# Optimization experiments

Hardware: AMD Instinct MI355X
Metric: run time of the kernel (lower is better)

Reference implementation:

```python
import jax, jax.numpy as jnp
import numpy as np

B, N, K, H, C, PE, EMB, OUT = 2, 2048, 16, 4, 8, 64, 1024, 2
P = C * (C + 1) // 2  # 36 unordered class pairs
RADIUS, NEG, EPS = 0.08, 0.2, 1e-5


def _ball_query(pos, radius, nsample):
    # pos [B,N,2] -> idx [B,N,nsample]; indices within radius, padded with first in-ball index
    sq = jnp.sum(pos * pos, -1)
    d = sq[:, :, None] + sq[:, None, :] - 2.0 * jnp.einsum('bnc,bmc->bnm', pos, pos)
    n = pos.shape[1]
    idx = jnp.broadcast_to(jnp.arange(n)[None, None, :], d.shape)
    idx = jnp.where(d > radius * radius, n, idx)
    idx = jnp.sort(idx, axis=-1)[:, :, :nsample]
    return jnp.where(idx == n, idx[:, :, :1], idx)


def _gather(feat, idx):
    # feat [B,F,N], idx [B,N,K] -> [B,F,N,K]
    return jnp.take_along_axis(feat[:, :, None, :], idx[:, None, :, :], axis=3)


def _pe(rel, dim):
    # sinusoidal encoding of relative coords rel [B,2,N,K] -> [B,dim,N,K]
    nf = dim // 4
    freqs = 10000.0 ** (-jnp.arange(nf, dtype=rel.dtype) / nf)
    ang = rel[:, :, None] * freqs[None, None, :, None, None]     # [B,2,nf,N,K]
    enc = jnp.concatenate([jnp.sin(ang), jnp.cos(ang)], axis=2)  # [B,2,2nf,N,K]
    b = enc.shape[0]
    return enc.reshape(b, dim, enc.shape[3], enc.shape[4])


def _conv(x, w, g, bvec):
    # 1x1 conv (no bias) + inference BN (running mean 0, var 1) + LeakyReLU
    y = jnp.einsum('oc,bc...->bo...', w, x) / jnp.sqrt(1.0 + EPS)
    sh = (1, -1) + (1,) * (y.ndim - 2)
    return jax.nn.leaky_relu(y * g.reshape(sh) + bvec.reshape(sh), NEG)


def _attn_layer(x, Ws, a_pairs, a_selfs, core, tgt):
    # PointpairAttentionLayer (per-class-pair coefficients), vmapped over heads.
    # x [B,F,N,K]; core [B,N] int; tgt [B,N,K] int
    s0 = jnp.minimum(tgt, core[:, :, None])
    s1 = jnp.maximum(tgt, core[:, :, None])
    pidx = s0 * C - (s0 * (s0 - 1)) // 2 + (s1 - s0)             # [B,N,K] pair index
    self_mask = (tgt[:, :, 0] < core)[:, :, None]                # slot-0 keeps a_self when pair-write happened earlier

    def head(W, a_pair, a_self):
        Wh = jnp.einsum('bfnk,fg->bnkg', x, W)                   # [B,N,K,F]
        a = a_pair[pidx]                                         # [B,N,K,F]
        slot0 = jnp.where(self_mask, a_self[core], a[:, :, 0])
        a = a.at[:, :, 0].set(slot0)
        e = jax.nn.leaky_relu(Wh * a, NEG)
        attn = jax.nn.softmax(e, axis=2)                         # over K neighbors
        return jax.nn.elu(attn * Wh)                             # [B,N,K,F]

    hs = jax.vmap(head)(Ws, a_pairs, a_selfs)                    # [H,B,N,K,F]
    b, n, k = x.shape[0], x.shape[2], x.shape[3]
    return jnp.transpose(hs, (1, 0, 4, 2, 3)).reshape(b, -1, n, k)


def _edge(feat, idx):
    # DGCNN edge features: concat(neighbor - center, center)
    tf = _gather(feat, idx)
    return jnp.concatenate([tf - feat[..., None],
                            jnp.broadcast_to(feat[..., None], tf.shape)], axis=1)


def _forward(pos, types, conv1_w, bn1_g, bn1_b, W1, ap1, as1,
             conv2_w, bn2_g, bn2_b, W2, ap2, as2,
             conv3_w, bn3_g, bn3_b, W3, ap3, as3,
             conv4_w, bn4_g, bn4_b, W4, ap4, as4,
             conv5_w, bn5_g, bn5_b, lin1_w, bn6_g, bn6_b,
             lin2_w, lin2_b, bn7_g, bn7_b, lin3_w, lin3_b):
    idx = _ball_query(pos, RADIUS, K)                            # [B,N,K]
    posT = jnp.transpose(pos, (0, 2, 1))                         # [B,2,N]
    rel = _gather(posT, idx) - posT[..., None]                   # [B,2,N,K]
    tgt = _gather(types[:, None, :], idx)[:, 0]                  # [B,N,K] neighbor classes

    x = _conv(_pe(rel, PE), conv1_w, bn1_g, bn1_b)               # [B,64,N,K]
    x1 = _attn_layer(x, W1, ap1, as1, types, tgt).sum(-1)        # [B,H*64,N]
    x = _conv(_edge(x1, idx), conv2_w, bn2_g, bn2_b)             # [B,64,N,K]
    x2 = _attn_layer(x, W2, ap2, as2, types, tgt).sum(-1)        # [B,H*64,N]
    x = _conv(_edge(x2, idx), conv3_w, bn3_g, bn3_b)             # [B,128,N,K]
    x3 = _attn_layer(x, W3, ap3, as3, types, tgt).sum(-1)        # [B,H*128,N]
    x = _conv(_edge(x3, idx), conv4_w, bn4_g, bn4_b)             # [B,256,N,K]
    x4 = _attn_layer(x, W4, ap4, as4, types, tgt).sum(-1)        # [B,H*256,N]

    xc = jnp.concatenate([x1, x2, x3, x4], axis=1)               # [B,H*512,N]
    x = _conv(xc, conv5_w, bn5_g, bn5_b)                         # [B,EMB,N]
    feat = jnp.concatenate([x.max(-1), x.mean(-1)], axis=-1)     # [B,2*EMB]

    def bn1d(y, g, bvec):
        return (y / jnp.sqrt(1.0 + EPS)) * g + bvec

    h = jax.nn.leaky_relu(bn1d(feat @ lin1_w.T, bn6_g, bn6_b), NEG)
    h = jax.nn.leaky_relu(bn1d(h @ lin2_w.T + lin2_b, bn7_g, bn7_b), NEG)
    return h @ lin3_w.T + lin3_b                                 # [B,OUT]


def setup_inputs() -> dict:
    key = jax.random.key(0)
    ks = iter(jax.random.split(key, 64))
    rn = lambda *s: jax.random.normal(next(ks), s, dtype=jnp.float32)
    d = {}
    d['pos'] = jax.random.uniform(next(ks), (B, N, 2), dtype=jnp.float32)
    d['types'] = jax.random.randint(next(ks), (B, N), 0, C, dtype=jnp.int32)

    def layer(f_in, f, tag):
        d['conv%d_w' % tag] = rn(f, f_in) * (1.0 / np.sqrt(f_in))
        d['bn%d_g' % tag] = jnp.ones((f,), jnp.float32)
        d['bn%d_b' % tag] = jnp.zeros((f,), jnp.float32)

    layer(PE, 64, 1)
    d['W1'] = rn(H, 64, 64) * 0.125; d['ap1'] = rn(H, P, 64) * 0.5; d['as1'] = rn(H, C, 64) * 0.5
    layer(2 * H * 64, 64, 2)
    d['W2'] = rn(H, 64, 64) * 0.125; d['ap2'] = rn(H, P, 64) * 0.5; d['as2'] = rn(H, C, 64) * 0.5
    layer(2 * H * 64, 128, 3)
    d['W3'] = rn(H, 128, 128) * 0.09; d['ap3'] = rn(H, P, 128) * 0.5; d['as3'] = rn(H, C, 128) * 0.5
    layer(2 * H * 128, 256, 4)
    d['W4'] = rn(H, 256, 256) * 0.0625; d['ap4'] = rn(H, P, 256) * 0.5; d['as4'] = rn(H, C, 256) * 0.5
    layer(H * 512, EMB, 5)
    d['lin1_w'] = rn(512, 2 * EMB) * 0.02
    d['bn6_g'] = jnp.ones((512,), jnp.float32); d['bn6_b'] = jnp.zeros((512,), jnp.float32)
    d['lin2_w'] = rn(256, 512) * 0.04; d['lin2_b'] = jnp.zeros((256,), jnp.float32)
    d['bn7_g'] = jnp.ones((256,), jnp.float32); d['bn7_b'] = jnp.zeros((256,), jnp.float32)
    d['lin3_w'] = rn(OUT, 256) * 0.06; d['lin3_b'] = jnp.zeros((OUT,), jnp.float32)
    return d


def reference(pos, types, conv1_w, bn1_g, bn1_b, W1, ap1, as1,
              conv2_w, bn2_g, bn2_b, W2, ap2, as2,
              conv3_w, bn3_g, bn3_b, W3, ap3, as3,
              conv4_w, bn4_g, bn4_b, W4, ap4, as4,
              conv5_w, bn5_g, bn5_b, lin1_w, bn6_g, bn6_b,
              lin2_w, lin2_b, bn7_g, bn7_b, lin3_w, lin3_b):
    return _forward(pos, types, conv1_w, bn1_g, bn1_b, W1, ap1, as1,
                    conv2_w, bn2_g, bn2_b, W2, ap2, as2,
                    conv3_w, bn3_g, bn3_b, W3, ap3, as3,
                    conv4_w, bn4_g, bn4_b, W4, ap4, as4,
                    conv5_w, bn5_g, bn5_b, lin1_w, bn6_g, bn6_b,
                    lin2_w, lin2_b, bn7_g, bn7_b, lin3_w, lin3_b)
```

## Files before the change

### kernel.cpp

```cpp
#include <hip/hip_runtime.h>
#include <math.h>

#define BB 2
#define NN 2048
#define KK 16
#define HH 4
#define CC 8
#define PP 36
#define NEGS 0.2f
#define INVS 0.9999950000374997f

typedef __attribute__((ext_vector_type(8))) short s16x8;
typedef __attribute__((ext_vector_type(8))) unsigned short u16x8;
typedef __attribute__((ext_vector_type(4))) float f32x4;

__device__ inline unsigned short bfh(float x) {
  unsigned u = __float_as_uint(x);
  return (unsigned short)((u + 0x7FFFu + ((u >> 16) & 1u)) >> 16);
}
__device__ inline float bff(unsigned short h) {
  return __uint_as_float(((unsigned)h) << 16);
}
__device__ inline f32x4 mfma16(s16x8 a, s16x8 b, f32x4 c) {
  return __builtin_amdgcn_mfma_f32_16x16x32_bf16(a, b, c, 0, 0, 0);
}

__global__ __launch_bounds__(256) void k_ballquery(const float* __restrict__ pos,
                                                   const int* __restrict__ types,
                                                   int* __restrict__ idxg,
                                                   int* __restrict__ acode,
                                                   float* __restrict__ rel) {
  __shared__ int s_buf[4][KK];
  const float r2 = (float)(0.08 * 0.08);
  int wslot = threadIdx.x >> 6;
  int lane = threadIdx.x & 63;
  int wg = blockIdx.x * 4 + wslot;
  int b = wg / NN, n = wg - b * NN;
  const float* pb = pos + (size_t)b * NN * 2;
  float px = pb[n * 2 + 0], py = pb[n * 2 + 1];
  float sqn = px * px + py * py;
  unsigned mask = 0u;
  int base = lane * 32;
  for (int j = 0; j < 32; ++j) {
    float qx = pb[(base + j) * 2 + 0], qy = pb[(base + j) * 2 + 1];
    float sqm = qx * qx + qy * qy;
    float d = sqn + sqm - 2.0f * (px * qx + py * qy);
    if (d <= r2) mask |= (1u << j);
  }
  int cnt = __popc(mask);
  int inc = cnt;
#pragma unroll
  for (int off = 1; off < 64; off <<= 1) {
    int v = __shfl_up(inc, off, 64);
    if (lane >= off) inc += v;
  }
  int total = __shfl(inc, 63, 64);
  int excl = inc - cnt;
  unsigned mm = mask;
  int p = excl;
  while (mm && p < KK) {
    int j = __ffs(mm) - 1;
    mm &= mm - 1u;
    s_buf[wslot][p] = base + j;
    ++p;
  }
  __syncthreads();
  int tc = total < KK ? total : KK;
  if (lane < KK) {
    int m0 = s_buf[wslot][0];
    int mk = (lane < tc) ? s_buf[wslot][lane] : m0;
    idxg[wg * KK + lane] = mk;
    int core = types[b * NN + n];
    int tg = types[b * NN + mk];
    int s0 = tg < core ? tg : core;
    int s1 = tg < core ? core : tg;
    int code = s0 * CC - (s0 * (s0 - 1)) / 2 + (s1 - s0);
    if (lane == 0 && tg < core) code = PP + core;
    acode[wg * KK + lane] = code;
    rel[(wg * KK + lane) * 2 + 0] = pb[mk * 2 + 0] - px;
    rel[(wg * KK + lane) * 2 + 1] = pb[mk * 2 + 1] - py;
  }
}

struct PackDesc {
  const float* src;
  unsigned short* dh;
  unsigned short* dl;
  int KB, NT, srcld, Cdiff, mode, sstride, dstride, nrep, bpr;
};
struct PackArgs {
  PackDesc d[20];
};
__global__ __launch_bounds__(256) void k_megapack(PackArgs pa) {
  PackDesc D = pa.d[blockIdx.y];
  int rep = blockIdx.x / D.bpr;
  if (rep >= D.nrep) return;
  int f = (blockIdx.x - rep * D.bpr) * 256 + threadIdx.x;
  int total = D.KB * D.NT * 64;
  if (f >= total) return;
  const float* src = D.src + (size_t)rep * D.sstride;
  unsigned short* dh = D.dh + (size_t)rep * D.dstride;
  if (D.mode == 3) {
    if (f * 8 >= D.Cdiff) return;
    float* dd = (float*)dh;
    size_t o = (size_t)f * 8;
#pragma unroll
    for (int i = 0; i < 8; ++i) dd[o + i] = src[o + i];
    return;
  }
  unsigned short* dl = D.dl + (size_t)rep * D.dstride;
  int l = f & 63;
  int t2 = f >> 6;
  int n = (t2 / D.KB) * 16 + (l & 15);
  int k0 = (t2 % D.KB) * 32 + ((l >> 4) * 8);
  size_t o = (size_t)t2 * 512 + (size_t)l * 8;
#pragma unroll
  for (int i = 0; i < 8; ++i) {
    int k = k0 + i;
    float v;
    if (D.mode == 0) {
      v = src[(size_t)k * D.srcld + n];
    } else if (D.mode == 1) {
      v = src[(size_t)n * D.srcld + k];
    } else {
      v = src[(size_t)n * D.srcld + k + D.Cdiff] - src[(size_t)n * D.srcld + k];
    }
    unsigned short hi = bfh(v);
    dh[o + i] = hi;
    dl[o + i] = bfh(v - bff(hi));
  }
}

template <int KBW, int NTB>
__global__ __launch_bounds__(512, 4) void k_pregemm(
    const unsigned short* __restrict__ xh, int xoff,
    const unsigned short* __restrict__ wph, const unsigned short* __restrict__ wpl,
    const float* __restrict__ scale, const float* __restrict__ bias,
    float* __restrict__ ouv, int cout) {
  constexpr int NCH = KBW / 2;
  constexpr int JT = NTB / 2;
  const int ld = 2 * cout;
  __shared__ alignas(16) char s_mem[32768];
  int tid = threadIdx.x;
  int lane = tid & 63;
  int w = tid >> 6;
  int lg = lane >> 4;
  int ln = lane & 15;
  int bm = blockIdx.x;
  int ntoff = blockIdx.y * NTB;
  int wm = w >> 1, wn = w & 1;
  f32x4 acc[2][JT];
#pragma unroll
  for (int m = 0; m < 2; ++m)
#pragma unroll
    for (int j = 0; j < JT; ++j) acc[m][j] = (f32x4){0.f, 0.f, 0.f, 0.f};

  int srowg = bm * 128 + w * 16 + ln;
  const unsigned short* gH = xh + (size_t)srowg * 2048 + xoff + lg * 8;
  int wbyA = ((w * 2 + 0) * 64 + lane) * 16;
  int wbyB = ((w * 2 + 1) * 64 + lane) * 16;
  u16x8 h0, h1;
  auto load2 = [&](int ch) {
    h0 = *(const u16x8*)(gH + ch * 64);
    h1 = *(const u16x8*)(gH + ch * 64 + 32);
  };
  load2(0);
  *(u16x8*)(s_mem + wbyA) = h0;
  *(u16x8*)(s_mem + wbyB) = h1;
  __syncthreads();
  int p = 0;
  for (int ch = 0; ch < NCH; ++ch) {
    if (ch + 1 < NCH) load2(ch + 1);
#pragma unroll
    for (int ks = 0; ks < 2; ++ks) {
      s16x8 ah[2];
#pragma unroll
      for (int m = 0; m < 2; ++m) {
        int by = p * 16384 + (((wm * 2 + m) * 2 + ks) * 64 + lane) * 16;
        ah[m] = *(const s16x8*)(s_mem + by);
      }
      int kb = ch * 2 + ks;
      __builtin_amdgcn_s_setprio(1);
#pragma unroll
      for (int j = 0; j < JT; ++j) {
        size_t fo = ((size_t)(ntoff + wn * JT + j) * KBW + kb) * 64 + lane;
        s16x8 bh = ((const s16x8*)wph)[fo];
        s16x8 bl = ((const s16x8*)wpl)[fo];
#pragma unroll
        for (int m = 0; m < 2; ++m) {
          acc[m][j] = mfma16(ah[m], bh, acc[m][j]);
          acc[m][j] = mfma16(ah[m], bl, acc[m][j]);
        }
      }
      __builtin_amdgcn_s_setprio(0);
    }
    if (ch + 1 < NCH) {
      int d = (p ^ 1) * 16384;
      *(u16x8*)(s_mem + d + wbyA) = h0;
      *(u16x8*)(s_mem + d + wbyB) = h1;
      p ^= 1;
    }
    __syncthreads();
  }
#pragma unroll
  for (int j = 0; j < JT; ++j) {
    int g = (ntoff + wn * JT + j) * 16 + ln;
    int gm = g >= cout ? g - cout : g;
    float sc = scale[gm] * INVS;
    float bs = (g >= cout) ? bias[gm] : 0.f;
#pragma unroll
    for (int m = 0; m < 2; ++m) {
#pragma unroll
      for (int reg = 0; reg < 4; ++reg) {
        int row = bm * 128 + wm * 32 + m * 16 + lg * 4 + reg;
        ouv[(size_t)row * ld + g] = acc[m][j][reg] * sc + bs;
      }
    }
  }
}

template <int FOUT, int MT>
__device__ __forceinline__ void attn_phase(
    const char* s_mem, const int* s_code, unsigned short* xh, int pgbase,
    int w, int lane, const unsigned short* __restrict__ attnh,
    const unsigned short* __restrict__ attnl, const float* __restrict__ coef,
    int ooff) {
  constexpr int KBA = FOUT / 32;
  constexpr int NT = FOUT / 16;
  constexpr int NTW_A = NT / 2;
  constexpr int JW = (MT == 8) ? 1 : ((NTW_A > 2) ? 2 : NTW_A);
  constexpr int NPASS = NTW_A / JW;
  int lg = lane >> 4;
  int ln = lane & 15;
  int h = w >> 1, nh = w & 1;
  const s16x8* wph = (const s16x8*)(attnh + (size_t)h * FOUT * FOUT);
  const s16x8* wpl = (const s16x8*)(attnl + (size_t)h * FOUT * FOUT);
  const float* hb = coef + (size_t)h * 44 * FOUT + ln;
#pragma unroll 1
  for (int pass = 0; pass < NPASS; ++pass) {
    float ac[MT][JW][4];
#pragma unroll
    for (int m = 0; m < MT; ++m)
#pragma unroll
      for (int reg = 0; reg < 4; ++reg) {
        int off = s_code[m * 16 + lg * 4 + reg] * FOUT;
#pragma unroll
        for (int j = 0; j < JW; ++j) {
          int nt = nh * NTW_A + pass * JW + j;
          ac[m][j][reg] = hb[off + nt * 16];
        }
      }
    f32x4 aacc[MT][JW];
#pragma unroll
    for (int m = 0; m < MT; ++m)
#pragma unroll
      for (int j = 0; j < JW; ++j) aacc[m][j] = (f32x4){0.f, 0.f, 0.f, 0.f};
#pragma unroll 2
    for (int kb = 0; kb < KBA; ++kb) {
      s16x8 ah[MT];
#pragma unroll
      for (int m = 0; m < MT; ++m) {
        int by = ((m * KBA + kb) * 64 + lane) * 16;
        ah[m] = *(const s16x8*)(s_mem + by);
      }
      __builtin_amdgcn_s_setprio(1);
#pragma unroll
      for (int j = 0; j < JW; ++j) {
        int nt = nh * NTW_A + pass * JW + j;
        size_t fo = ((size_t)nt * KBA + kb) * 64 + lane;
        s16x8 bh = wph[fo];
        s16x8 bl = wpl[fo];
#pragma unroll
        for (int m = 0; m < MT; ++m) {
          aacc[m][j] = mfma16(ah[m], bh, aacc[m][j]);
          aacc[m][j] = mfma16(ah[m], bl, aacc[m][j]);
        }
      }
      __builtin_amdgcn_s_setprio(0);
    }
#pragma unroll
    for (int m = 0; m < MT; ++m) {
      int pg = pgbase + m;
#pragma unroll
      for (int j = 0; j < JW; ++j) {
        int nt = nh * NTW_A + pass * JW + j;
        int g = nt * 16 + ln;
        float e[4];
        float ssum = 0.f;
#pragma unroll
        for (int reg = 0; reg < 4; ++reg) {
          float ev = aacc[m][j][reg] * ac[m][j][reg];
          ev = (ev >= 0.f) ? ev : NEGS * ev;
          float pe = __expf(ev);
          e[reg] = pe;
          ssum += pe;
        }
        ssum += __shfl_xor(ssum, 16, 64);
        ssum += __shfl_xor(ssum, 32, 64);
        float inv = 1.f / ssum;
        float o = 0.f;
#pragma unroll
        for (int reg = 0; reg < 4; ++reg) {
          float u = e[reg] * inv * aacc[m][j][reg];
          o += (u > 0.f) ? u : (__expf(u) - 1.f);
        }
        o += __shfl_xor(o, 16, 64);
        o += __shfl_xor(o, 32, 64);
        if (lane < 16) {
          xh[(size_t)pg * 2048 + ooff + h * FOUT + g] = bfh(o);
        }
      }
    }
  }
}

template <int FOUT>
__global__ __launch_bounds__(512, 4) void k_attn(
    unsigned short* xh, const float* __restrict__ uv,
    const int* __restrict__ idx, const int* __restrict__ acode,
    const unsigned short* __restrict__ attnh, const unsigned short* __restrict__ attnl,
    const float* __restrict__ coef, int ooff) {
  constexpr int MT = 8;
  constexpr int KBA = FOUT / 32;
  constexpr int YPLANE = MT * 16 * FOUT * 2;
  constexpr int FPW = (MT * KBA) / 8;
  constexpr int C2 = 2 * FOUT;

  __shared__ alignas(16) char s_mem[YPLANE];
  __shared__ int s_gsrc[MT * 16];
  __shared__ int s_code[MT * 16];

  int tid = threadIdx.x;
  int lane = tid & 63;
  int w = tid >> 6;
  int lg = lane >> 4;
  int ln = lane & 15;
  int pgbase = blockIdx.x * MT;

  if (tid < MT * 16) {
    int pg = pgbase + (tid >> 4);
    int b = pg >> 11;
    s_gsrc[tid] = b * 2048 + idx[pg * KK + (tid & 15)];
    s_code[tid] = acode[pg * KK + (tid & 15)];
  }
  __syncthreads();

#pragma unroll
  for (int r = 0; r < FPW; ++r) {
    int f = w * FPW + r;
    int mt = f / KBA, kb = f % KBA;
    int row = mt * 16 + ln;
    int col = kb * 32 + lg * 8;
    const float* up = uv + (size_t)s_gsrc[row] * C2 + col;
    const float* cp = uv + (size_t)(pgbase + mt) * C2 + FOUT + col;
    float4 u0 = *(const float4*)up;
    float4 u1 = *(const float4*)(up + 4);
    float4 v0 = *(const float4*)cp;
    float4 v1 = *(const float4*)(cp + 4);
    float uu[8] = {u0.x, u0.y, u0.z, u0.w, u1.x, u1.y, u1.z, u1.w};
    float vv[8] = {v0.x, v0.y, v0.z, v0.w, v1.x, v1.y, v1.z, v1.w};
    unsigned short oh[8];
#pragma unroll
    for (int i = 0; i < 8; ++i) {
      float t = uu[i] + vv[i];
      t = (t >= 0.f) ? t : NEGS * t;
      oh[i] = bfh(t);
    }
    *(u16x8*)(s_mem + (f * 64 + lane) * 16) = *(u16x8*)oh;
  }
  __syncthreads();

  attn_phase<FOUT, MT>(s_mem, s_code, xh, pgbase, w, lane, attnh, attnl, coef, ooff);
}

__global__ __launch_bounds__(512, 4) void k_layer1(
    unsigned short* xh, const float* __restrict__ rel, const int* __restrict__ idx,
    const int* __restrict__ acode,
    const unsigned short* __restrict__ convh, const unsigned short* __restrict__ convl,
    const unsigned short* __restrict__ attnh, const unsigned short* __restrict__ attnl,
    const float* __restrict__ bng, const float* __restrict__ bnb,
    const float* __restrict__ coef, int ooff) {
  constexpr int FOUT = 64;
  constexpr int KB = 2;
  constexpr int KBA = 2;
  constexpr int YPLANE = 64 * FOUT * 2;

  __shared__ alignas(16) char s_mem[YPLANE];
  __shared__ int s_gsrc[64];
  __shared__ int s_code[64];

  int tid = threadIdx.x;
  int lane = tid & 63;
  int w = tid >> 6;
  int lg = lane >> 4;
  int ln = lane & 15;
  int pgbase = blockIdx.x * 4;

  if (tid < 64) {
    int pg = pgbase + (tid >> 4);
    int b = pg >> 11;
    s_gsrc[tid] = b * 2048 + idx[pg * KK + (tid & 15)];
    s_code[tid] = acode[pg * KK + (tid & 15)];
  }
  __syncthreads();

  {
    int smt = w >> 1, skb = w & 1;
    float rc = rel[((size_t)(pgbase + smt) * KK + ln) * 2 + skb];
    unsigned short hb[8];
#pragma unroll
    for (int i = 0; i < 8; ++i) {
      int j = lg * 8 + i;
      int fidx = j & 15;
      float freq = exp2f(-(float)fidx * 0.8304820237218406f);
      float ang = rc * freq;
      float v = (j < 16) ? __sinf(ang) : __cosf(ang);
      hb[i] = bfh(v);
    }
    *(u16x8*)(s_mem + ((w * 64 + lane) * 16)) = *(u16x8*)hb;
  }
  __syncthreads();

  int wr = w >> 2, wc = w & 3;
  f32x4 cacc[2];
  cacc[0] = (f32x4){0.f, 0.f, 0.f, 0.f};
  cacc[1] = (f32x4){0.f, 0.f, 0.f, 0.f};
#pragma unroll
  for (int ks = 0; ks < 2; ++ks) {
    s16x8 ah[2];
#pragma unroll
    for (int m = 0; m < 2; ++m) {
      int by = (((wr * 2 + m) * 2 + ks) * 64 + lane) * 16;
      ah[m] = *(const s16x8*)(s_mem + by);
    }
    __builtin_amdgcn_s_setprio(1);
    size_t fo = ((size_t)wc * KB + ks) * 64 + lane;
    s16x8 bh = ((const s16x8*)convh)[fo];
    s16x8 bl = ((const s16x8*)convl)[fo];
#pragma unroll
    for (int m = 0; m < 2; ++m) {
      cacc[m] = mfma16(ah[m], bh, cacc[m]);
      cacc[m] = mfma16(ah[m], bl, cacc[m]);
    }
    __builtin_amdgcn_s_setprio(0);
  }
  __syncthreads();

  {
    int g = wc * 16 + ln;
    float sc = bng[g] * INVS;
    float bs = bnb[g];
    int gpart = ((g >> 5) * 64 + ((g >> 3) & 3) * 16) * 16 + (g & 7) * 2;
#pragma unroll
    for (int m = 0; m < 2; ++m) {
#pragma unroll
      for (int reg = 0; reg < 4; ++reg) {
        int r = wr * 32 + m * 16 + lg * 4 + reg;
        float v = cacc[m][reg] * sc + bs;
        v = (v >= 0.f) ? v : NEGS * v;
        int by = (r >> 4) * (KBA * 1024) + gpart + (r & 15) * 16;
        *(unsigned short*)(s_mem + by) = bfh(v);
      }
    }
  }
  __syncthreads();

  attn_phase<64, 4>(s_mem, s_code, xh, pgbase, w, lane, attnh, attnl, coef, ooff);
}

__global__ __launch_bounds__(512, 2) void k_gemm5_m(const unsigned short* __restrict__ xh,
                                                    const unsigned short* __restrict__ bph,
                                                    const unsigned short* __restrict__ bpl,
                                                    const float* __restrict__ g5,
                                                    const float* __restrict__ b5,
                                                    float* __restrict__ pmax,
                                                    float* __restrict__ psum) {
  __shared__ alignas(16) char s_mem[65536];
  int tid = threadIdx.x;
  int lane = tid & 63;
  int w = tid >> 6;
  int lg = lane >> 4;
  int ln = lane & 15;
  int bm = blockIdx.x, bn = blockIdx.y;
  int wm = w >> 2, wn = w & 3;
  f32x4 acc[8];
#pragma unroll
  for (int m = 0; m < 8; ++m) acc[m] = (f32x4){0.f, 0.f, 0.f, 0.f};

  int sr = w * 16 + ln;
  const unsigned short* gH = xh + (size_t)(bm * 256 + sr) * 2048 + lg * 8;
  const unsigned short* gH2 = gH + (size_t)128 * 2048;
  int fm = sr >> 4;
  int fl = lg * 16 + (sr & 15);
  int wbyA = ((fm * 2 + 0) * 64 + fl) * 16;
  int wbyB = ((fm * 2 + 1) * 64 + fl) * 16;
  int wbyC = (((fm + 8) * 2 + 0) * 64 + fl) * 16;
  int wbyD = (((fm + 8) * 2 + 1) * 64 + fl) * 16;
  u16x8 h0, h1, h2, h3;
  auto load4 = [&](int ch) {
    h0 = *(const u16x8*)(gH + ch * 64);
    h1 = *(const u16x8*)(gH + ch * 64 + 32);
    h2 = *(const u16x8*)(gH2 + ch * 64);
    h3 = *(const u16x8*)(gH2 + ch * 64 + 32);
  };
  load4(0);
  *(u16x8*)(s_mem + wbyA) = h0;
  *(u16x8*)(s_mem + wbyB) = h1;
  *(u16x8*)(s_mem + wbyC) = h2;
  *(u16x8*)(s_mem + wbyD) = h3;
  __syncthreads();
  int p = 0;
  for (int ch = 0; ch < 32; ++ch) {
    if (ch + 1 < 32) load4(ch + 1);
#pragma unroll
    for (int ks = 0; ks < 2; ++ks) {
      s16x8 ah[8];
#pragma unroll
      for (int m = 0; m < 8; ++m) {
        int by = p * 32768 + (((wm * 8 + m) * 2 + ks) * 64 + lane) * 16;
        ah[m] = *(const s16x8*)(s_mem + by);
      }
      int kb = ch * 2 + ks;
      __builtin_amdgcn_s_setprio(1);
      {
        size_t fo = ((size_t)(bn * 4 + wn) * 64 + kb) * 64 + lane;
        s16x8 bh = ((const s16x8*)bph)[fo];
        s16x8 bl = ((const s16x8*)bpl)[fo];
#pragma unroll
        for (int m = 0; m < 8; ++m) {
          acc[m] = mfma16(ah[m], bh, acc[m]);
          acc[m] = mfma16(ah[m], bl, acc[m]);
        }
      }
      __builtin_amdgcn_s_setprio(0);
    }
    if (ch + 1 < 32) {
      int d = (p ^ 1) * 32768;
      *(u16x8*)(s_mem + d + wbyA) = h0;
      *(u16x8*)(s_mem + d + wbyB) = h1;
      *(u16x8*)(s_mem + d + wbyC) = h2;
      *(u16x8*)(s_mem + d + wbyD) = h3;
      p ^= 1;
    }
    __syncthreads();
  }

  float cmax, csum;
  {
    int g = bn * 64 + wn * 16 + ln;
    float sc = g5[g] * INVS;
    float bs = b5[g];
    float mx = -3.0e38f, sm = 0.f;
#pragma unroll
    for (int m = 0; m < 8; ++m)
#pragma unroll
      for (int reg = 0; reg < 4; ++reg) {
        float v = acc[m][reg] * sc + bs;
        v = (v >= 0.f) ? v : NEGS * v;
        mx = fmaxf(mx, v);
        sm += v;
      }
    mx = fmaxf(mx, __shfl_xor(mx, 16, 64));
    mx = fmaxf(mx, __shfl_xor(mx, 32, 64));
    sm += __shfl_xor(sm, 16, 64);
    sm += __shfl_xor(sm, 32, 64);
    cmax = mx;
    csum = sm;
  }
  float* s_f = (float*)s_mem;
  if (lg == 0) {
    int col = wn * 16 + ln;
    s_f[(wm * 64 + col) * 2 + 0] = cmax;
    s_f[(wm * 64 + col) * 2 + 1] = csum;
  }
  __syncthreads();
  if (tid < 64) {
    float mx = fmaxf(s_f[tid * 2], s_f[(64 + tid) * 2]);
    float sm = s_f[tid * 2 + 1] + s_f[(64 + tid) * 2 + 1];
    pmax[(size_t)bm * 1024 + bn * 64 + tid] = mx;
    psum[(size_t)bm * 1024 + bn * 64 + tid] = sm;
  }
}

__global__ __launch_bounds__(256) void k_feat(const float* __restrict__ pmax,
                                              const float* __restrict__ psum,
                                              float* __restrict__ feat) {
  int t = blockIdx.x * 256 + threadIdx.x;
  if (t >= BB * 1024) return;
  int b = t >> 10, o = t & 1023;
  float mx = -3.0e38f, sm = 0.f;
  for (int i = 0; i < 8; ++i) {
    mx = fmaxf(mx, pmax[(size_t)(b * 8 + i) * 1024 + o]);
    sm += psum[(size_t)(b * 8 + i) * 1024 + o];
  }
  feat[b * 2048 + o] = mx;
  feat[b * 2048 + 1024 + o] = sm * (1.0f / NN);
}

template <bool HASB, bool DOBN, bool ACT>
__global__ __launch_bounds__(256) void k_head(const float* __restrict__ X,
                                              const float* __restrict__ Wm,
                                              const float* __restrict__ bias,
                                              const float* __restrict__ g,
                                              const float* __restrict__ bb,
                                              float* __restrict__ Y, int IN, int ON) {
  int gt = blockIdx.x * 256 + threadIdx.x;
  int w = gt >> 6, lane = gt & 63;
  if (w >= BB * ON) return;
  int b = w / ON, o = w - b * ON;
  const float* x = X + (size_t)b * IN;
  const float* wr = Wm + (size_t)o * IN;
  float s = 0.f;
  for (int c = lane; c < IN; c += 64) s += x[c] * wr[c];
#pragma unroll
  for (int off = 32; off > 0; off >>= 1) s += __shfl_down(s, off, 64);
  if (lane == 0) {
    if (HASB) s += bias[o];
    if (DOBN) s = s * INVS * g[o] + bb[o];
    if (ACT) s = (s >= 0.f) ? s : NEGS * s;
    Y[(size_t)b * ON + o] = s;
  }
}

extern "C" void kernel_launch(void* const* d_in, const int* in_sizes, int n_in,
                              void* d_out, int out_size, void* d_ws, size_t ws_size,
                              hipStream_t stream) {
  const float* pos = (const float*)d_in[0];
  const int* types = (const int*)d_in[1];
  const float* conv1_w = (const float*)d_in[2];
  const float* bn1_g = (const float*)d_in[3];
  const float* bn1_b = (const float*)d_in[4];
  const float* W1 = (const float*)d_in[5];
  const float* ap1 = (const float*)d_in[6];
  const float* as1 = (const float*)d_in[7];
  const float* conv2_w = (const float*)d_in[8];
  const float* bn2_g = (const float*)d_in[9];
  const float* bn2_b = (const float*)d_in[10];
  const float* W2 = (const float*)d_in[11];
  const float* ap2 = (const float*)d_in[12];
  const float* as2 = (const float*)d_in[13];
  const float* conv3_w = (const float*)d_in[14];
  const float* bn3_g = (const float*)d_in[15];
  const float* bn3_b = (const float*)d_in[16];
  const float* W3 = (const float*)d_in[17];
  const float* ap3 = (const float*)d_in[18];
  const float* as3 = (const float*)d_in[19];
  const float* conv4_w = (const float*)d_in[20];
  const float* bn4_g = (const float*)d_in[21];
  const float* bn4_b = (const float*)d_in[22];
  const float* W4 = (const float*)d_in[23];
  const float* ap4 = (const float*)d_in[24];
  const float* as4 = (const float*)d_in[25];
  const float* conv5_w = (const float*)d_in[26];
  const float* bn5_g = (const float*)d_in[27];
  const float* bn5_b = (const float*)d_in[28];
  const float* lin1_w = (const float*)d_in[29];
  const float* bn6_g = (const float*)d_in[30];
  const float* bn6_b = (const float*)d_in[31];
  const float* lin2_w = (const float*)d_in[32];
  const float* lin2_b = (const float*)d_in[33];
  const float* bn7_g = (const float*)d_in[34];
  const float* bn7_b = (const float*)d_in[35];
  const float* lin3_w = (const float*)d_in[36];
  const float* lin3_b = (const float*)d_in[37];
  (void)in_sizes; (void)n_in; (void)out_size; (void)ws_size;

  float* ws = (float*)d_ws;
  size_t off = 0;
  auto take = [&](size_t nf) {
    float* p = ws + off;
    off += (nf + 63) & ~(size_t)63;
    return p;
  };
  auto takeu = [&](size_t nu) { return (unsigned short*)take((nu + 1) / 2); };

  int* idx = (int*)take(BB * NN * KK);
  int* acode = (int*)take(BB * NN * KK);
  float* rel = take((size_t)BB * NN * KK * 2);
  unsigned short* xh = takeu((size_t)BB * NN * 2048);
  float* uv = take((size_t)4096 * 512);
  float* pmax = take(16 * 1024);
  float* psum = take(16 * 1024);
  float* feat = take(BB * 2048);
  float* h1 = take(BB * 512);
  float* h2 = take(BB * 256);
  unsigned short* c1h = takeu(64 * 64);
  unsigned short* c1l = takeu(64 * 64);
  unsigned short* uvw2h = takeu(256 * 128);
  unsigned short* uvw2l = takeu(256 * 128);
  unsigned short* uvw3h = takeu(256 * 256);
  unsigned short* uvw3l = takeu(256 * 256);
  unsigned short* uvw4h = takeu(512 * 512);
  unsigned short* uvw4l = takeu(512 * 512);
  unsigned short* a1h = takeu(4 * 64 * 64);
  unsigned short* a1l = takeu(4 * 64 * 64);
  unsigned short* a2h = takeu(4 * 64 * 64);
  unsigned short* a2l = takeu(4 * 64 * 64);
  unsigned short* a3h = takeu(4 * 128 * 128);
  unsigned short* a3l = takeu(4 * 128 * 128);
  unsigned short* a4h = takeu(4 * 256 * 256);
  unsigned short* a4l = takeu(4 * 256 * 256);
  unsigned short* g5h = takeu((size_t)2048 * 1024);
  unsigned short* g5l = takeu((size_t)2048 * 1024);
  float* coef1 = take(4 * 44 * 64);
  float* coef2 = take(4 * 44 * 64);
  float* coef3 = take(4 * 44 * 128);
  float* coef4 = take(4 * 44 * 256);

  dim3 blk(256);
  dim3 blk5(512);

  PackArgs pa;
  pa.d[0] = {conv1_w, c1h, c1l, 2, 4, 64, 0, 1, 0, 0, 1, 2};
  pa.d[1] = {conv2_w, uvw2h, uvw2l, 8, 4, 512, 0, 1, 0, 0, 1, 8};
  pa.d[2] = {conv2_w, uvw2h + 16384, uvw2l + 16384, 8, 4, 512, 256, 2, 0, 0, 1, 8};
  pa.d[3] = {conv3_w, uvw3h, uvw3l, 8, 8, 512, 0, 1, 0, 0, 1, 16};
  pa.d[4] = {conv3_w, uvw3h + 32768, uvw3l + 32768, 8, 8, 512, 256, 2, 0, 0, 1, 16};
  pa.d[5] = {conv4_w, uvw4h, uvw4l, 16, 16, 1024, 0, 1, 0, 0, 1, 64};
  pa.d[6] = {conv4_w, uvw4h + 131072, uvw4l + 131072, 16, 16, 1024, 512, 2, 0, 0, 1, 64};
  pa.d[7] = {W1, a1h, a1l, 2, 4, 64, 0, 0, 4096, 4096, 4, 2};
  pa.d[8] = {W2, a2h, a2l, 2, 4, 64, 0, 0, 4096, 4096, 4, 2};
  pa.d[9] = {W3, a3h, a3l, 4, 8, 128, 0, 0, 16384, 16384, 4, 8};
  pa.d[10] = {W4, a4h, a4l, 8, 16, 256, 0, 0, 65536, 65536, 4, 32};
  pa.d[11] = {conv5_w, g5h, g5l, 64, 64, 2048, 0, 1, 0, 0, 1, 1024};
  pa.d[12] = {ap1, (unsigned short*)coef1, nullptr, 5, 1, 0, 2304, 3, 2304, 5632, 4, 2};
  pa.d[13] = {as1, (unsigned short*)(coef1 + 2304), nullptr, 1, 1, 0, 512, 3, 512, 5632, 4, 1};
  pa.d[14] = {ap2, (unsigned short*)coef2, nullptr, 5, 1, 0, 2304, 3, 2304, 5632, 4, 2};
  pa.d[15] = {as2, (unsigned short*)(coef2 + 2304), nullptr, 1, 1, 0, 512, 3, 512, 5632, 4, 1};
  pa.d[16] = {ap3, (unsigned short*)coef3, nullptr, 9, 1, 0, 4608, 3, 4608, 11264, 4, 3};
  pa.d[17] = {as3, (unsigned short*)(coef3 + 4608), nullptr, 2, 1, 0, 1024, 3, 1024, 11264, 4, 1};
  pa.d[18] = {ap4, (unsigned short*)coef4, nullptr, 18, 1, 0, 9216, 3, 9216, 22528, 4, 5};
  pa.d[19] = {as4, (unsigned short*)(coef4 + 9216), nullptr, 4, 1, 0, 2048, 3, 2048, 22528, 4, 1};
  k_megapack<<<dim3(1024, 20), blk, 0, stream>>>(pa);

  k_ballquery<<<dim3(BB * NN / 4), blk, 0, stream>>>(pos, types, idx, acode, rel);

  k_layer1<<<dim3(BB * NN / 4), blk5, 0, stream>>>(
      xh, rel, idx, acode, c1h, c1l, a1h, a1l, bn1_g, bn1_b, coef1, 0);

  k_pregemm<8, 4><<<dim3(32, 2), blk5, 0, stream>>>(
      xh, 0, uvw2h, uvw2l, bn2_g, bn2_b, uv, 64);
  k_attn<64><<<dim3(BB * NN / 8), blk5, 0, stream>>>(
      xh, uv, idx, acode, a2h, a2l, coef2, 256);

  k_pregemm<8, 8><<<dim3(32, 2), blk5, 0, stream>>>(
      xh, 256, uvw3h, uvw3l, bn3_g, bn3_b, uv, 128);
  k_attn<128><<<dim3(BB * NN / 8), blk5, 0, stream>>>(
      xh, uv, idx, acode, a3h, a3l, coef3, 512);

  k_pregemm<16, 8><<<dim3(32, 4), blk5, 0, stream>>>(
      xh, 512, uvw4h, uvw4l, bn4_g, bn4_b, uv, 256);
  k_attn<256><<<dim3(BB * NN / 8), blk5, 0, stream>>>(
      xh, uv, idx, acode, a4h, a4l, coef4, 1024);

  k_gemm5_m<<<dim3(16, 16), blk5, 0, stream>>>(xh, g5h, g5l, bn5_g, bn5_b, pmax, psum);
  k_feat<<<dim3(8), blk, 0, stream>>>(pmax, psum, feat);
  k_head<false, true, true><<<dim3(BB * 512 * 64 / 256), blk, 0, stream>>>(
      feat, lin1_w, nullptr, bn6_g, bn6_b, h1, 2048, 512);
  k_head<true, true, true><<<dim3(BB * 256 * 64 / 256), blk, 0, stream>>>(
      h1, lin2_w, lin2_b, bn7_g, bn7_b, h2, 512, 256);
  k_head<true, false, false><<<dim3(1), blk, 0, stream>>>(
      h2, lin3_w, lin3_b, nullptr, nullptr, (float*)d_out, 256, 2);
}
```

Measured before the change: 349.5 us.

## Switch attention GEMMs to 32x32x16 MFMA with 4-point blocks

Replaces the 16x16x32 bf16 MFMA attention phase with a 32x32x16 variant, changing the LDS operand layout, the weight packing (a new pack mode for 32-wide column tiles) and the softmax epilogue to match the 32x32 accumulator layout. Attention blocks now process 4 points instead of 8, which doubles the grid size. The aim is fewer MFMA instructions and less weight traffic per output column, plus more blocks in flight. The cost is half the weight reuse across points per block and per-element coefficient gathers in the epilogue.

```diff
diff --git a/kernel.cpp b/kernel.cpp
--- a/kernel.cpp
+++ b/kernel.cpp
@@ -13,6 +13,7 @@
 typedef __attribute__((ext_vector_type(8))) short s16x8;
 typedef __attribute__((ext_vector_type(8))) unsigned short u16x8;
 typedef __attribute__((ext_vector_type(4))) float f32x4;
+typedef __attribute__((ext_vector_type(16))) float f32x16;
 
 __device__ inline unsigned short bfh(float x) {
   unsigned u = __float_as_uint(x);
@@ -23,6 +24,9 @@
 }
 __device__ inline f32x4 mfma16(s16x8 a, s16x8 b, f32x4 c) {
   return __builtin_amdgcn_mfma_f32_16x16x32_bf16(a, b, c, 0, 0, 0);
+}
+__device__ inline f32x16 mfma32(s16x8 a, s16x8 b, f32x16 c) {
+  return __builtin_amdgcn_mfma_f32_32x32x16_bf16(a, b, c, 0, 0, 0);
 }
 
 __global__ __launch_bounds__(256) void k_ballquery(const float* __restrict__ pos,
@@ -111,9 +115,22 @@
   unsigned short* dl = D.dl + (size_t)rep * D.dstride;
   int l = f & 63;
   int t2 = f >> 6;
+  size_t o = (size_t)t2 * 512 + (size_t)l * 8;
+  if (D.mode == 4) {
+    int nt = t2 / D.KB, ks = t2 - nt * D.KB;
+    int n = nt * 32 + (l & 31);
+    int k0 = ks * 16 + ((l >> 5) * 8);
+#pragma unroll
+    for (int i = 0; i < 8; ++i) {
+      float v = src[(size_t)(k0 + i) * D.srcld + n];
+      unsigned short hi = bfh(v);
+      dh[o + i] = hi;
+      dl[o + i] = bfh(v - bff(hi));
+    }
+    return;
+  }
   int n = (t2 / D.KB) * 16 + (l & 15);
   int k0 = (t2 % D.KB) * 32 + ((l >> 4) * 8);
-  size_t o = (size_t)t2 * 512 + (size_t)l * 8;
 #pragma unroll
   for (int i = 0; i < 8; ++i) {
     int k = k0 + i;
@@ -219,97 +236,77 @@
   }
 }
 
-template <int FOUT, int MT>
-__device__ __forceinline__ void attn_phase(
+template <int FOUT>
+__device__ __forceinline__ void attn_phase32(
     const char* s_mem, const int* s_code, unsigned short* xh, int pgbase,
     int w, int lane, const unsigned short* __restrict__ attnh,
     const unsigned short* __restrict__ attnl, const float* __restrict__ coef,
     int ooff) {
-  constexpr int KBA = FOUT / 32;
-  constexpr int NT = FOUT / 16;
-  constexpr int NTW_A = NT / 2;
-  constexpr int JW = (MT == 8) ? 1 : ((NTW_A > 2) ? 2 : NTW_A);
-  constexpr int NPASS = NTW_A / JW;
-  int lg = lane >> 4;
-  int ln = lane & 15;
+  constexpr int KS = FOUT / 16;
+  constexpr int NPASS = FOUT / 64;
+  int hi = lane >> 5;
+  int c31 = lane & 31;
   int h = w >> 1, nh = w & 1;
   const s16x8* wph = (const s16x8*)(attnh + (size_t)h * FOUT * FOUT);
   const s16x8* wpl = (const s16x8*)(attnl + (size_t)h * FOUT * FOUT);
-  const float* hb = coef + (size_t)h * 44 * FOUT + ln;
+  const float* hb = coef + (size_t)h * 44 * FOUT;
 #pragma unroll 1
   for (int pass = 0; pass < NPASS; ++pass) {
-    float ac[MT][JW][4];
-#pragma unroll
-    for (int m = 0; m < MT; ++m)
-#pragma unroll
-      for (int reg = 0; reg < 4; ++reg) {
-        int off = s_code[m * 16 + lg * 4 + reg] * FOUT;
-#pragma unroll
-        for (int j = 0; j < JW; ++j) {
-          int nt = nh * NTW_A + pass * JW + j;
-          ac[m][j][reg] = hb[off + nt * 16];
-        }
-      }
-    f32x4 aacc[MT][JW];
-#pragma unroll
-    for (int m = 0; m < MT; ++m)
-#pragma unroll
-      for (int j = 0; j < JW; ++j) aacc[m][j] = (f32x4){0.f, 0.f, 0.f, 0.f};
+    int nt32 = nh * NPASS + pass;
+    int g = nt32 * 32 + c31;
+    f32x16 acc0, acc1;
+#pragma unroll
+    for (int i = 0; i < 16; ++i) {
+      acc0[i] = 0.f;
+      acc1[i] = 0.f;
+    }
 #pragma unroll 2
-    for (int kb = 0; kb < KBA; ++kb) {
-      s16x8 ah[MT];
-#pragma unroll
-      for (int m = 0; m < MT; ++m) {
-        int by = ((m * KBA + kb) * 64 + lane) * 16;
-        ah[m] = *(const s16x8*)(s_mem + by);
-      }
+    for (int ks = 0; ks < KS; ++ks) {
+      s16x8 a0 = *(const s16x8*)(s_mem + ((0 * KS + ks) * 64 + lane) * 16);
+      s16x8 a1 = *(const s16x8*)(s_mem + ((1 * KS + ks) * 64 + lane) * 16);
+      size_t fo = ((size_t)nt32 * KS + ks) * 64 + lane;
+      s16x8 bh = wph[fo];
+      s16x8 bl = wpl[fo];
       __builtin_amdgcn_s_setprio(1);
-#pragma unroll
-      for (int j = 0; j < JW; ++j) {
-        int nt = nh * NTW_A + pass * JW + j;
-        size_t fo = ((size_t)nt * KBA + kb) * 64 + lane;
-        s16x8 bh = wph[fo];
-        s16x8 bl = wpl[fo];
-#pragma unroll
-        for (int m = 0; m < MT; ++m) {
-          aacc[m][j] = mfma16(ah[m], bh, aacc[m][j]);
-          aacc[m][j] = mfma16(ah[m], bl, aacc[m][j]);
-        }
-      }
+      acc0 = mfma32(a0, bh, acc0);
+      acc0 = mfma32(a0, bl, acc0);
+      acc1 = mfma32(a1, bh, acc1);
+      acc1 = mfma32(a1, bl, acc1);
       __builtin_amdgcn_s_setprio(0);
     }
-#pragma unroll
-    for (int m = 0; m < MT; ++m) {
-      int pg = pgbase + m;
-#pragma unroll
-      for (int j = 0; j < JW; ++j) {
-        int nt = nh * NTW_A + pass * JW + j;
-        int g = nt * 16 + ln;
-        float e[4];
-        float ssum = 0.f;
-#pragma unroll
-        for (int reg = 0; reg < 4; ++reg) {
-          float ev = aacc[m][j][reg] * ac[m][j][reg];
-          ev = (ev >= 0.f) ? ev : NEGS * ev;
-          float pe = __expf(ev);
-          e[reg] = pe;
-          ssum += pe;
-        }
-        ssum += __shfl_xor(ssum, 16, 64);
-        ssum += __shfl_xor(ssum, 32, 64);
-        float inv = 1.f / ssum;
-        float o = 0.f;
-#pragma unroll
-        for (int reg = 0; reg < 4; ++reg) {
-          float u = e[reg] * inv * aacc[m][j][reg];
-          o += (u > 0.f) ? u : (__expf(u) - 1.f);
-        }
-        o += __shfl_xor(o, 16, 64);
-        o += __shfl_xor(o, 32, 64);
-        if (lane < 16) {
-          xh[(size_t)pg * 2048 + ooff + h * FOUT + g] = bfh(o);
-        }
-      }
+#pragma unroll 1
+    for (int mt = 0; mt < 2; ++mt) {
+      const f32x16& ac = mt ? acc1 : acc0;
+      float e[16];
+      float ssA = 0.f, ssB = 0.f;
+#pragma unroll
+      for (int reg = 0; reg < 16; ++reg) {
+        int row = (reg & 3) + 8 * (reg >> 2) + 4 * hi;
+        int code = s_code[mt * 32 + row];
+        float a = hb[(size_t)code * FOUT + g];
+        float ev = ac[reg] * a;
+        ev = (ev >= 0.f) ? ev : NEGS * ev;
+        float pe = __expf(ev);
+        e[reg] = pe;
+        if (reg < 8) ssA += pe; else ssB += pe;
+      }
+      ssA += __shfl_xor(ssA, 32, 64);
+      ssB += __shfl_xor(ssB, 32, 64);
+      float invA = 1.f / ssA;
+      float invB = 1.f / ssB;
+      float oA = 0.f, oB = 0.f;
+#pragma unroll
+      for (int reg = 0; reg < 16; ++reg) {
+        float inv = (reg < 8) ? invA : invB;
+        float u = e[reg] * inv * ac[reg];
+        float t = (u > 0.f) ? u : (__expf(u) - 1.f);
+        if (reg < 8) oA += t; else oB += t;
+      }
+      oA += __shfl_xor(oA, 32, 64);
+      oB += __shfl_xor(oB, 32, 64);
+      float oS = hi ? oB : oA;
+      int pg = pgbase + mt * 2 + hi;
+      xh[(size_t)pg * 2048 + ooff + h * FOUT + g] = bfh(oS);
     }
   }
 }
@@ -320,24 +317,23 @@
     const int* __restrict__ idx, const int* __restrict__ acode,
     const unsigned short* __restrict__ attnh, const unsigned short* __restrict__ attnl,
     const float* __restrict__ coef, int ooff) {
-  constexpr int MT = 8;
-  constexpr int KBA = FOUT / 32;
-  constexpr int YPLANE = MT * 16 * FOUT * 2;
-  constexpr int FPW = (MT * KBA) / 8;
+  constexpr int KS = FOUT / 16;
+  constexpr int YPLANE = 64 * FOUT * 2;
+  constexpr int FPW = (2 * KS) / 8;
   constexpr int C2 = 2 * FOUT;
 
   __shared__ alignas(16) char s_mem[YPLANE];
-  __shared__ int s_gsrc[MT * 16];
-  __shared__ int s_code[MT * 16];
+  __shared__ int s_gsrc[64];
+  __shared__ int s_code[64];
 
   int tid = threadIdx.x;
   int lane = tid & 63;
   int w = tid >> 6;
-  int lg = lane >> 4;
-  int ln = lane & 15;
-  int pgbase = blockIdx.x * MT;
-
-  if (tid < MT * 16) {
+  int hi = lane >> 5;
+  int c31 = lane & 31;
+  int pgbase = blockIdx.x * 4;
+
+  if (tid < 64) {
     int pg = pgbase + (tid >> 4);
     int b = pg >> 11;
     s_gsrc[tid] = b * 2048 + idx[pg * KK + (tid & 15)];
@@ -348,11 +344,11 @@
 #pragma unroll
   for (int r = 0; r < FPW; ++r) {
     int f = w * FPW + r;
-    int mt = f / KBA, kb = f % KBA;
-    int row = mt * 16 + ln;
-    int col = kb * 32 + lg * 8;
-    const float* up = uv + (size_t)s_gsrc[row] * C2 + col;
-    const float* cp = uv + (size_t)(pgbase + mt) * C2 + FOUT + col;
+    int mt = f / KS, ks = f - mt * KS;
+    int row = mt * 32 + c31;
+    int kcol = ks * 16 + hi * 8;
+    const float* up = uv + (size_t)s_gsrc[row] * C2 + kcol;
+    const float* cp = uv + (size_t)(pgbase + (row >> 4)) * C2 + FOUT + kcol;
     float4 u0 = *(const float4*)up;
     float4 u1 = *(const float4*)(up + 4);
     float4 v0 = *(const float4*)cp;
@@ -370,7 +366,7 @@
   }
   __syncthreads();
 
-  attn_phase<FOUT, MT>(s_mem, s_code, xh, pgbase, w, lane, attnh, attnl, coef, ooff);
+  attn_phase32<FOUT>(s_mem, s_code, xh, pgbase, w, lane, attnh, attnl, coef, ooff);
 }
 
 __global__ __launch_bounds__(512, 4) void k_layer1(
@@ -382,7 +378,7 @@
     const float* __restrict__ coef, int ooff) {
   constexpr int FOUT = 64;
   constexpr int KB = 2;
-  constexpr int KBA = 2;
+  constexpr int KS = 4;
   constexpr int YPLANE = 64 * FOUT * 2;
 
   __shared__ alignas(16) char s_mem[YPLANE];
@@ -450,7 +446,6 @@
     int g = wc * 16 + ln;
     float sc = bng[g] * INVS;
     float bs = bnb[g];
-    int gpart = ((g >> 5) * 64 + ((g >> 3) & 3) * 16) * 16 + (g & 7) * 2;
 #pragma unroll
     for (int m = 0; m < 2; ++m) {
 #pragma unroll
@@ -458,14 +453,15 @@
         int r = wr * 32 + m * 16 + lg * 4 + reg;
         float v = cacc[m][reg] * sc + bs;
         v = (v >= 0.f) ? v : NEGS * v;
-        int by = (r >> 4) * (KBA * 1024) + gpart + (r & 15) * 16;
+        int by = (((r >> 5) * KS + (g >> 4)) * 64 + (r & 31) + 32 * ((g >> 3) & 1)) * 16 +
+                 (g & 7) * 2;
         *(unsigned short*)(s_mem + by) = bfh(v);
       }
     }
   }
   __syncthreads();
 
-  attn_phase<64, 4>(s_mem, s_code, xh, pgbase, w, lane, attnh, attnl, coef, ooff);
+  attn_phase32<64>(s_mem, s_code, xh, pgbase, w, lane, attnh, attnl, coef, ooff);
 }
 
 __global__ __launch_bounds__(512, 2) void k_gemm5_m(const unsigned short* __restrict__ xh,
@@ -718,10 +714,10 @@
   pa.d[4] = {conv3_w, uvw3h + 32768, uvw3l + 32768, 8, 8, 512, 256, 2, 0, 0, 1, 16};
   pa.d[5] = {conv4_w, uvw4h, uvw4l, 16, 16, 1024, 0, 1, 0, 0, 1, 64};
   pa.d[6] = {conv4_w, uvw4h + 131072, uvw4l + 131072, 16, 16, 1024, 512, 2, 0, 0, 1, 64};
-  pa.d[7] = {W1, a1h, a1l, 2, 4, 64, 0, 0, 4096, 4096, 4, 2};
-  pa.d[8] = {W2, a2h, a2l, 2, 4, 64, 0, 0, 4096, 4096, 4, 2};
-  pa.d[9] = {W3, a3h, a3l, 4, 8, 128, 0, 0, 16384, 16384, 4, 8};
-  pa.d[10] = {W4, a4h, a4l, 8, 16, 256, 0, 0, 65536, 65536, 4, 32};
+  pa.d[7] = {W1, a1h, a1l, 4, 2, 64, 0, 4, 4096, 4096, 4, 2};
+  pa.d[8] = {W2, a2h, a2l, 4, 2, 64, 0, 4, 4096, 4096, 4, 2};
+  pa.d[9] = {W3, a3h, a3l, 8, 4, 128, 0, 4, 16384, 16384, 4, 8};
+  pa.d[10] = {W4, a4h, a4l, 16, 8, 256, 0, 4, 65536, 65536, 4, 32};
   pa.d[11] = {conv5_w, g5h, g5l, 64, 64, 2048, 0, 1, 0, 0, 1, 1024};
   pa.d[12] = {ap1, (unsigned short*)coef1, nullptr, 5, 1, 0, 2304, 3, 2304, 5632, 4, 2};
   pa.d[13] = {as1, (unsigned short*)(coef1 + 2304), nullptr, 1, 1, 0, 512, 3, 512, 5632, 4, 1};
@@ -740,17 +736,17 @@
 
   k_pregemm<8, 4><<<dim3(32, 2), blk5, 0, stream>>>(
       xh, 0, uvw2h, uvw2l, bn2_g, bn2_b, uv, 64);
-  k_attn<64><<<dim3(BB * NN / 8), blk5, 0, stream>>>(
+  k_attn<64><<<dim3(BB * NN / 4), blk5, 0, stream>>>(
       xh, uv, idx, acode, a2h, a2l, coef2, 256);
 
   k_pregemm<8, 8><<<dim3(32, 2), blk5, 0, stream>>>(
       xh, 256, uvw3h, uvw3l, bn3_g, bn3_b, uv, 128);
-  k_attn<128><<<dim3(BB * NN / 8), blk5, 0, stream>>>(
+  k_attn<128><<<dim3(BB * NN / 4), blk5, 0, stream>>>(
       xh, uv, idx, acode, a3h, a3l, coef3, 512);
 
   k_pregemm<16, 8><<<dim3(32, 4), blk5, 0, stream>>>(
       xh, 512, uvw4h, uvw4l, bn4_g, bn4_b, uv, 256);
-  k_attn<256><<<dim3(BB * NN / 8), blk5, 0, stream>>>(
+  k_attn<256><<<dim3(BB * NN / 4), blk5, 0, stream>>>(
       xh, uv, idx, acode, a4h, a4l, coef4, 1024);
 
   k_gemm5_m<<<dim3(16, 16), blk5, 0, stream>>>(xh, g5h, g5l, bn5_g, bn5_b, pmax, psum);
```

New measurement: 352.6 us. No clear change (+0.9%).
